# Performance work log

Hardware: AMD Instinct MI355X
Metric: run time of the kernel (lower is better)

## Reference

```python
import jax, jax.numpy as jnp
import numpy as np

K = 40  # GravNetConv k (hardcoded in PFNet7.forward's conv1)

def lrelu(x):
    # LeakyReLU(negative_slope=0.5)
    return jnp.where(x >= 0, x, 0.5 * x)

def lin(x, W, b=None):
    y = x @ W
    return y + b if b is not None else y


def setup_inputs() -> dict:
    key = jax.random.key(0)
    ks = jax.random.split(key, 24)
    N = 16384
    inp = {}
    inp["x0"] = jax.random.normal(ks[0], (N, 12), jnp.float32)
    inp["ygen"] = jax.random.normal(ks[1], (N, 6), jnp.float32)
    inp["ycand"] = jax.random.normal(ks[2], (N, 6), jnp.float32)
    inp["ygen_id"] = jax.random.randint(ks[3], (N,), 0, 6)
    inp["ycand_id"] = jax.random.randint(ks[4], (N,), 0, 6)

    def lp(k, din, dout):  # torch Linear default init (uniform +/- 1/sqrt(fan_in))
        s = float(1.0 / np.sqrt(din))
        kw, kb = jax.random.split(k)
        W = jax.random.uniform(kw, (din, dout), jnp.float32, -s, s)
        b = jax.random.uniform(kb, (dout,), jnp.float32, -s, s)
        return W, b

    inp["n1W0"], inp["n1b0"] = lp(ks[5], 12, 64)
    inp["n1W1"], inp["n1b1"] = lp(ks[6], 64, 64)
    inp["n1W2"], inp["n1b2"] = lp(ks[7], 64, 12)
    # GravNetConv: lin_s (space, 8), lin_h (propagate, 22), lin_out (12 + 2*22 -> 64)
    inp["gWs"], inp["gbs"] = lp(ks[8], 12, 8)
    inp["gWh"], inp["gbh"] = lp(ks[9], 12, 22)
    inp["gWo"], inp["gbo"] = lp(ks[10], 56, 64)
    # GraphConv: lin_rel (with bias), lin_root (no bias, PyG convention)
    inp["c2Wrel"], inp["c2brel"] = lp(ks[11], 64, 64)
    inp["c2Wroot"] = lp(ks[12], 64, 64)[0]
    inp["n2W0"], inp["n2b0"] = lp(ks[13], 64, 126)
    inp["n2W1"], inp["n2b1"] = lp(ks[14], 126, 126)
    inp["n2W2"], inp["n2b2"] = lp(ks[15], 126, 126)
    inp["n2W3"], inp["n2b3"] = lp(ks[16], 126, 6)
    inp["n3W0"], inp["n3b0"] = lp(ks[17], 82, 126)
    inp["n3W1"], inp["n3b1"] = lp(ks[18], 126, 126)
    inp["n3W2"], inp["n3b2"] = lp(ks[19], 126, 126)
    inp["n3W3"], inp["n3b3"] = lp(ks[20], 126, 6)
    return inp


def reference(x0, ygen, ycand, ygen_id, ycand_id,
              n1W0, n1b0, n1W1, n1b1, n1W2, n1b2,
              gWs, gbs, gWh, gbh, gWo, gbo,
              c2Wrel, c2brel, c2Wroot,
              n2W0, n2b0, n2W1, n2b1, n2W2, n2b2, n2W3, n2b3,
              n3W0, n3b0, n3W1, n3b1, n3W2, n3b2, n3W3, n3b3):
    N = x0.shape[0]
    # nn1 encoder
    x = lrelu(lin(x0, n1W0, n1b0))
    x = lrelu(lin(x, n1W1, n1b1))
    x = lrelu(lin(x, n1W2, n1b2))            # [N,12]
    # ---- GravNetConv: dynamic kNN graph in learned 8-dim space ----
    s = lin(x, gWs, gbs)                     # [N,8] spatial coords
    h = lin(x, gWh, gbh)                     # [N,22] propagated features
    sq = jnp.sum(s * s, axis=1)
    d2 = sq[:, None] + sq[None, :] - 2.0 * (s @ s.T)   # [N,N] squared dists
    ar = jnp.arange(N)
    d2 = d2.at[ar, ar].set(jnp.inf)          # knn_graph loop=False: no self edges
    negd2, idx = jax.lax.top_k(-d2, K)       # [N,K] k nearest neighbors
    w = jnp.exp(10.0 * negd2)                # edge_weight = exp(-10 * d^2)
    msg = h[idx] * w[..., None]              # [N,K,22] gathered messages
    agg = jnp.concatenate([msg.mean(axis=1), msg.max(axis=1)], axis=-1)  # [N,44]
    x = lin(jnp.concatenate([agg, x], axis=-1), gWo, gbo)  # [N,64]
    # ---- GraphConv on the same kNN graph (add-aggregation, edge-weighted) ----
    nbr = jnp.sum(x[idx] * w[..., None], axis=1)  # [N,64]
    x = lin(nbr, c2Wrel, c2brel) + x @ c2Wroot     # [N,64]
    # nn2: class id head
    y = lrelu(lin(x, n2W0, n2b0))
    y = lrelu(lin(y, n2W1, n2b1))
    y = lrelu(lin(y, n2W2, n2b2))
    cand_ids = lrelu(lin(y, n2W3, n2b3))     # [N,6]
    z = jnp.concatenate([x, cand_ids, x0], axis=-1)  # [N,82]
    z = lrelu(lin(z, n3W0, n3b0))
    z = lrelu(lin(z, n3W1, n3b1))
    z = lrelu(lin(z, n3W2, n3b2))
    cand_p4 = lrelu(lin(z, n3W3, n3b3))      # [N,6]
    return (cand_ids, cand_p4, ygen_id, ygen, ycand_id, ycand)
```

## Files before the change

### kernel.cpp

```cpp
#include <hip/hip_runtime.h>
#include <math.h>

static constexpr int KNN = 40;

__device__ __forceinline__ float lrelu_f(float v){ return v >= 0.f ? v : 0.5f*v; }

typedef _Float16 half8 __attribute__((ext_vector_type(8)));
typedef float    f32x4 __attribute__((ext_vector_type(4)));

__device__ __forceinline__ void gload16(const void* g, void* l){
    __builtin_amdgcn_global_load_lds((const __attribute__((address_space(1))) void*)g,
                                     (__attribute__((address_space(3))) void*)l, 16, 0, 0);
}

#define PAD_OFF_GWS   0
#define PAD_OFF_GWH   192
#define PAD_OFF_N1W2  576
#define PAD_OFF_N2W3  1600
#define PAD_OFF_N3W3  3616
#define PAD_TOTAL     5632

#define T_N2W0  0
#define T_N2W1  8192
#define T_N2W2  24576
#define T_N3W0  40960
#define T_N3W1  53248
#define T_N3W2  69632
#define T_TOTAL 86016

__global__ void pad_all(const float* gWs,const float* gWh,const float* n1W2,
                        const float* n2W3,const float* n3W3,
                        const float* n2W0,const float* n2W1,const float* n2W2,
                        const float* n3W0,const float* n3W1,const float* n3W2,
                        float* __restrict__ wp, _Float16* __restrict__ wt)
{
    int i = blockIdx.x*blockDim.x + threadIdx.x;
    if (i < PAD_TOTAL) {
        const float* src; int cols, sh, off;
        if      (i < PAD_OFF_GWH)  { src=gWs;  cols=8;  sh=4; off=PAD_OFF_GWS;  }
        else if (i < PAD_OFF_N1W2) { src=gWh;  cols=22; sh=5; off=PAD_OFF_GWH;  }
        else if (i < PAD_OFF_N2W3) { src=n1W2; cols=12; sh=4; off=PAD_OFF_N1W2; }
        else if (i < PAD_OFF_N3W3) { src=n2W3; cols=6;  sh=4; off=PAD_OFF_N2W3; }
        else                       { src=n3W3; cols=6;  sh=4; off=PAD_OFF_N3W3; }
        int li = i - off;
        int r = li >> sh, c = li & ((1<<sh)-1);
        wp[i] = (c < cols) ? src[r*cols + c] : 0.f;
        return;
    }
    int j = i - PAD_TOTAL;
    if (j >= T_TOTAL) return;
    const float* src; int KP, K, off;
    if      (j < T_N2W1) { src=n2W0; KP=64;  K=64;  off=T_N2W0; }
    else if (j < T_N2W2) { src=n2W1; KP=128; K=126; off=T_N2W1; }
    else if (j < T_N3W0) { src=n2W2; KP=128; K=126; off=T_N2W2; }
    else if (j < T_N3W1) { src=n3W0; KP=96;  K=82;  off=T_N3W0; }
    else if (j < T_N3W2) { src=n3W1; KP=128; K=126; off=T_N3W1; }
    else                 { src=n3W2; KP=128; K=126; off=T_N3W2; }
    int li = j - off;
    int n = li / KP, k = li - n*KP;
    float v = (n < 126 && k < K) ? src[k*126 + n] : 0.f;
    wt[j] = (_Float16)v;
}

template<int K, int NOUT, int WPITCH, bool RELU, int NTH>
__device__ __forceinline__
void lin8(const float* __restrict__ Xs, int xpitch,
          const float* __restrict__ W, const float* __restrict__ Bv,
          float* __restrict__ Y, int ypitch, int tid)
{
    constexpr int NP  = ((NOUT+7)/8)*8;
    constexpr int NCG = NP/8;
    constexpr int NW  = NTH/64;
    const int lane = tid & 63;
    for (int g0 = tid >> 6; g0 < NCG; g0 += NW) {
        const int cg = __builtin_amdgcn_readfirstlane(g0);
        float acc[8];
        #pragma unroll
        for (int j=0;j<8;++j){ int c=cg*8+j; acc[j] = (c < NOUT) ? Bv[c] : 0.f; }
        const float* xrow = &Xs[(long)lane*xpitch];
        const float* wp = &W[cg*8];
        #pragma unroll 4
        for (int k=0;k<K;++k){
            const float xv = xrow[k];
            const float4* w4 = reinterpret_cast<const float4*>(wp + (long)k*WPITCH);
            float4 a = w4[0], b = w4[1];
            acc[0]=fmaf(xv,a.x,acc[0]); acc[1]=fmaf(xv,a.y,acc[1]);
            acc[2]=fmaf(xv,a.z,acc[2]); acc[3]=fmaf(xv,a.w,acc[3]);
            acc[4]=fmaf(xv,b.x,acc[4]); acc[5]=fmaf(xv,b.y,acc[5]);
            acc[6]=fmaf(xv,b.z,acc[6]); acc[7]=fmaf(xv,b.w,acc[7]);
        }
        #pragma unroll
        for (int j=0;j<8;++j){
            int c = cg*8 + j;
            if (c < NOUT){ float v = acc[j]; if (RELU) v = lrelu_f(v); Y[(long)lane*ypitch + c] = v; }
        }
    }
    __syncthreads();
}

template<int K, int NOUT, int WPITCH, int NTH>
__device__ __forceinline__
void lin8_dual(const float* __restrict__ Xs, int xp, const float* __restrict__ X2s, int xp2,
               const float* __restrict__ W, const float* __restrict__ Bv, const float* __restrict__ W2,
               float* __restrict__ Y, int ypitch, int tid)
{
    constexpr int NP  = ((NOUT+7)/8)*8;
    constexpr int NCG = NP/8;
    constexpr int NW  = NTH/64;
    const int lane = tid & 63;
    for (int g0 = tid >> 6; g0 < NCG; g0 += NW) {
        const int cg = __builtin_amdgcn_readfirstlane(g0);
        float acc[8];
        #pragma unroll
        for (int j=0;j<8;++j){ int c=cg*8+j; acc[j] = (c < NOUT) ? Bv[c] : 0.f; }
        {
            const float* xrow = &Xs[(long)lane*xp];
            const float* wp = &W[cg*8];
            #pragma unroll 4
            for (int k=0;k<K;++k){
                const float xv = xrow[k];
                const float4* w4 = reinterpret_cast<const float4*>(wp + (long)k*WPITCH);
                float4 a = w4[0], b = w4[1];
                acc[0]=fmaf(xv,a.x,acc[0]); acc[1]=fmaf(xv,a.y,acc[1]);
                acc[2]=fmaf(xv,a.z,acc[2]); acc[3]=fmaf(xv,a.w,acc[3]);
                acc[4]=fmaf(xv,b.x,acc[4]); acc[5]=fmaf(xv,b.y,acc[5]);
                acc[6]=fmaf(xv,b.z,acc[6]); acc[7]=fmaf(xv,b.w,acc[7]);
            }
        }
        {
            const float* xrow = &X2s[(long)lane*xp2];
            const float* wp = &W2[cg*8];
            #pragma unroll 4
            for (int k=0;k<K;++k){
                const float xv = xrow[k];
                const float4* w4 = reinterpret_cast<const float4*>(wp + (long)k*WPITCH);
                float4 a = w4[0], b = w4[1];
                acc[0]=fmaf(xv,a.x,acc[0]); acc[1]=fmaf(xv,a.y,acc[1]);
                acc[2]=fmaf(xv,a.z,acc[2]); acc[3]=fmaf(xv,a.w,acc[3]);
                acc[4]=fmaf(xv,b.x,acc[4]); acc[5]=fmaf(xv,b.y,acc[5]);
                acc[6]=fmaf(xv,b.z,acc[6]); acc[7]=fmaf(xv,b.w,acc[7]);
            }
        }
        #pragma unroll
        for (int j=0;j<8;++j){
            int c = cg*8 + j;
            if (c < NOUT) Y[(long)lane*ypitch + c] = acc[j];
        }
    }
    __syncthreads();
}

__global__ __launch_bounds__(256)
void f1_encoder(const float* __restrict__ x0, const float* __restrict__ wp,
                const float* n1W0,const float* n1b0,const float* n1W1,const float* n1b1,
                const float* n1b2, const float* gbs, const float* gbh,
                float* __restrict__ x12g,
                _Float16* __restrict__ SA16, _Float16* __restrict__ SB16 ,
                float* __restrict__ hg )
{
    __shared__ float A1[64*65], A2[64*65], Ss[64*9];
    const int tid = threadIdx.x;
    const long row0 = (long)blockIdx.x*64;
    lin8<12,64,64,true,256>(x0+row0*12,12, n1W0, n1b0, A1,65, tid);
    lin8<64,64,64,true,256>(A1,65, n1W1, n1b1, A2,65, tid);
    lin8<64,12,16,true,256>(A2,65, wp+PAD_OFF_N1W2, n1b2, A1,13, tid);
    for (int i=tid;i<64*12;i+=256){ int r=i/12,c=i-r*12; x12g[(row0+r)*12+c]=A1[r*13+c]; }
    lin8<12,8,16,false,256>(A1,13, wp+PAD_OFF_GWS, gbs, Ss,9, tid);
    lin8<12,22,32,false,256>(A1,13, wp+PAD_OFF_GWH, gbh, hg+row0*32,32, tid);
    if (tid < 64) {
        const long node = row0 + tid;
        float sv[8]; float nq = 0.f;
        #pragma unroll
        for (int k=0;k<8;++k){ float v=Ss[tid*9+k]; sv[k]=v; nq=fmaf(v,v,nq); }
        _Float16 ch[8], clo[8];
        #pragma unroll
        for (int k=0;k<8;++k){ ch[k]=(_Float16)sv[k]; clo[k]=(_Float16)(sv[k]-(float)ch[k]); }
        _Float16 nh = (_Float16)nq, nl = (_Float16)(nq-(float)nh);
        const _Float16 one = (_Float16)1.f, zero = (_Float16)0.f;
        half8 a0,a1,a2,b0,b2;
        #pragma unroll
        for (int k=0;k<8;++k){
            a0[k]=ch[k]; a1[k]=clo[k]; a2[k]=ch[k];
            b0[k]=(_Float16)(-2.f*(float)ch[k]);
            b2[k]=(_Float16)(-2.f*(float)clo[k]);
        }
        half8 a3 = {nh, nl, one, one, zero, zero, zero, zero};
        half8 b3 = {one, one, nh, nl, zero, zero, zero, zero};
        half8* ap = (half8*)&SA16[(size_t)node*32];
        ap[0]=a0; ap[1]=a1; ap[2]=a2; ap[3]=a3;
        half8* bp = (half8*)&SB16[(size_t)node*40];
        bp[0]=b0; bp[1]=b0; bp[2]=b2; bp[3]=b3;
        bp[4]=half8{zero,zero,zero,zero,zero,zero,zero,zero};
    }
}

template<int C>
__device__ __forceinline__ unsigned dpp_umin(unsigned x){
    unsigned y = (unsigned)__builtin_amdgcn_update_dpp((int)x, (int)x, C, 0xf, 0xf, false);
    return x < y ? x : y;
}
__device__ __forceinline__ unsigned wave_umin64(unsigned x){
    x = dpp_umin<0x111>(x);
    x = dpp_umin<0x112>(x);
    x = dpp_umin<0x114>(x);
    x = dpp_umin<0x118>(x);
    x = dpp_umin<0x142>(x);
    x = dpp_umin<0x143>(x);
    return x;
}
__device__ __forceinline__ unsigned med3_u32(unsigned a, unsigned b, unsigned c){
    unsigned d;
    asm("v_med3_u32 %0, %1, %2, %3" : "=v"(d) : "v"(a), "v"(b), "v"(c));
    return d;
}

__global__ __launch_bounds__(512)
void knn_mfma(const _Float16* __restrict__ SA, const _Float16* __restrict__ SB,
              int* __restrict__ idx_out, float* __restrict__ w_out, int N)
{
    __shared__ __align__(16) _Float16 SBl[2][256*40];
    unsigned (*MRG)[128] = reinterpret_cast<unsigned(*)[128]>(&SBl[0][0]);
    const int tid  = threadIdx.x;
    const int lane = tid & 63;
    const int w    = tid >> 6;
    const int g    = w >> 2, qt = w & 3;
    const int col  = lane & 15, kg = lane >> 4;
    const int qb   = blockIdx.x*32 + g*16;
    const int qtile = qb >> 8;
    const int rhs0  = (qb & 255) + kg*4;

    half8 afrag = *(const half8*)&SA[(size_t)(qb + col)*32 + kg*8];
    unsigned s0[4], s1[4];
    #pragma unroll
    for (int r=0;r<4;++r){ s0[r]=0xFFFFFFFFu; s1[r]=0xFFFFFFFFu; }

    const int NT = N >> 8;
    {
        const char* gp = (const char*)SB;
        gload16(gp + (size_t)tid*16,        &SBl[0][(size_t)tid*8]);
        gload16(gp + (size_t)(tid+512)*16,  &SBl[0][(size_t)(tid+512)*8]);
        if (tid < 256) gload16(gp + (size_t)(tid+1024)*16, &SBl[0][(size_t)(tid+1024)*8]);
    }
    __syncthreads();
    #pragma unroll 1
    for (int t = 0; t < NT; ++t) {
        const int cur = t & 1;
        if (t+1 < NT) {
            const char* gp = (const char*)(SB + (size_t)(t+1)*256*40);
            _Float16* lp = SBl[cur^1];
            gload16(gp + (size_t)tid*16,        &lp[(size_t)tid*8]);
            gload16(gp + (size_t)(tid+512)*16,  &lp[(size_t)(tid+512)*8]);
            if (tid < 256) gload16(gp + (size_t)(tid+1024)*16, &lp[(size_t)(tid+1024)*8]);
        }
        const _Float16* tb = SBl[cur];
        if (t != qtile) {
            #pragma unroll
            for (int c3=0;c3<4;++c3){
                const int cl_ = (qt*4+c3)*16 + col;
                half8 b = *(const half8*)&tb[cl_*40 + kg*8];
                f32x4 acc = {0.f,0.f,0.f,0.f};
                acc = __builtin_amdgcn_mfma_f32_16x16x32_f16(afrag, b, acc, 0, 0, 0);
                const unsigned ib = (unsigned)((t<<2)|c3);
                #pragma unroll
                for (int r=0;r<4;++r){
                    float d2 = fmaxf(acc[r], 0.f);
                    unsigned key = (__float_as_uint(d2) & 0xFFFFFF00u) | ib;
                    unsigned lo = s0[r] < key ? s0[r] : key;
                    s1[r] = med3_u32(s0[r], s1[r], key);
                    s0[r] = lo;
                }
            }
        } else {
            #pragma unroll
            for (int c3=0;c3<4;++c3){
                const int cl_ = (qt*4+c3)*16 + col;
                half8 b = *(const half8*)&tb[cl_*40 + kg*8];
                f32x4 acc = {0.f,0.f,0.f,0.f};
                acc = __builtin_amdgcn_mfma_f32_16x16x32_f16(afrag, b, acc, 0, 0, 0);
                const unsigned ib = (unsigned)((t<<2)|c3);
                #pragma unroll
                for (int r=0;r<4;++r){
                    float d2 = fmaxf(acc[r], 0.f);
                    unsigned key = (__float_as_uint(d2) & 0xFFFFFF00u) | ib;
                    if (cl_ == rhs0 + r) key = 0xFFFFFFFFu;
                    unsigned lo = s0[r] < key ? s0[r] : key;
                    s1[r] = med3_u32(s0[r], s1[r], key);
                    s0[r] = lo;
                }
            }
        }
        __syncthreads();
    }

    #pragma unroll
    for (int r=0;r<4;++r){
        const int qloc = g*16 + kg*4 + r;
        MRG[qloc][qt*32 + col*2    ] = s0[r];
        MRG[qloc][qt*32 + col*2 + 1] = s1[r];
    }
    __syncthreads();

    const int myqt = lane >> 4, mycol = lane & 15;
    for (int qi=0; qi<4; ++qi){
        const int qloc = w*4 + qi;
        const long q = (long)blockIdx.x*32 + qloc;
        unsigned k0 = MRG[qloc][2*lane], k1 = MRG[qloc][2*lane+1];
        #pragma unroll 1
        for (int p=0;p<KNN;++p){
            unsigned lmin = k0 < k1 ? k0 : k1;
            unsigned red = wave_umin64(lmin);
            unsigned gm = (unsigned)__builtin_amdgcn_readlane((int)red, 63);
            unsigned long long bal = __ballot(lmin == gm);
            int owner = __ffsll((long long)bal) - 1;
            if (lane == owner){
                const int tt = (int)((gm>>2)&63u);
                const int c3 = (int)(gm & 3u);
                const int cand = tt*256 + (myqt*4+c3)*16 + mycol;
                const float d2 = __uint_as_float(gm & 0xFFFFFF00u);
                idx_out[q*KNN+p] = cand;
                w_out[q*KNN+p]   = expf(-10.f*d2);
                if (k0 == gm) k0 = k1;
                k1 = 0xFFFFFFFFu;
            }
        }
    }
}

__global__ __launch_bounds__(512)
void f2_agg(const float* __restrict__ hg , const int* __restrict__ idx,
            const float* __restrict__ wgt, const float* __restrict__ x12g,
            const float* gWo, const float* gbo, float* __restrict__ xg)
{
    __shared__ int   IDs[64*40];
    __shared__ float Wt[64*40];
    __shared__ float AGG[64*57];
    const int tid = threadIdx.x;
    const long row0 = (long)blockIdx.x*64;
    for (int i=tid;i<64*40;i+=512){ int r=i/40,k=i-r*40;
        IDs[i]=idx[(row0+r)*40+k]; Wt[i]=wgt[(row0+r)*40+k]; }
    for (int i=tid;i<64*12;i+=512){ int r=i/12,c=i-r*12; AGG[r*57+44+c]=x12g[(row0+r)*12+c]; }
    __syncthreads();
    {
        const int r = tid & 63, g = tid >> 6;
        const int f0 = g*4;
        const int nf = (f0 < 22) ? ((22-f0) < 4 ? (22-f0) : 4) : 0;
        float sm[4], mx[4];
        #pragma unroll
        for (int u=0;u<4;++u){ sm[u]=0.f; mx[u]=-INFINITY; }
        if (nf > 0) {
            #pragma unroll 1
            for (int k=0;k<40;++k){
                int j = IDs[r*40+k]; float wv = Wt[r*40+k];
                float4 h0 = *reinterpret_cast<const float4*>(&hg[(long)j*32 + f0]);
                float hv[4] = {h0.x,h0.y,h0.z,h0.w};
                #pragma unroll
                for (int u=0;u<4;++u){ float m = hv[u]*wv; sm[u]+=m; mx[u]=fmaxf(mx[u],m); }
            }
            #pragma unroll
            for (int u=0;u<4;++u) if (u<nf){ AGG[r*57+f0+u]=sm[u]*(1.f/40.f); AGG[r*57+22+f0+u]=mx[u]; }
        }
    }
    __syncthreads();
    lin8<56,64,64,false,512>(AGG,57, gWo, gbo, xg+row0*64,64, tid);
}

__global__ __launch_bounds__(512)
void f3_graphconv(const float* __restrict__ xgin, const int* __restrict__ idx,
                  const float* __restrict__ wgt,
                  const float* c2Wrel, const float* c2brel, const float* c2Wroot,
                  float* __restrict__ xc)
{
    __shared__ int   IDs[64*40];
    __shared__ float Wt[64*40];
    __shared__ float NB[64*65], XGs[64*65];
    const int tid = threadIdx.x;
    const long row0 = (long)blockIdx.x*64;
    for (int i=tid;i<64*40;i+=512){ int r=i/40,k=i-r*40;
        IDs[i]=idx[(row0+r)*40+k]; Wt[i]=wgt[(row0+r)*40+k]; }
    for (int i=tid;i<64*64;i+=512){ int r=i>>6,c=i&63; XGs[r*65+c]=xgin[(row0+r)*64+c]; }
    __syncthreads();
    {
        const int r = tid & 63, g = tid >> 6;
        float acc[8];
        #pragma unroll
        for (int j=0;j<8;++j) acc[j]=0.f;
        #pragma unroll 1
        for (int k=0;k<40;++k){
            int j = IDs[r*40+k]; float wv = Wt[r*40+k];
            const float4* xp = reinterpret_cast<const float4*>(&xgin[(long)j*64 + g*8]);
            float4 v0 = xp[0], v1 = xp[1];
            acc[0]=fmaf(v0.x,wv,acc[0]); acc[1]=fmaf(v0.y,wv,acc[1]);
            acc[2]=fmaf(v0.z,wv,acc[2]); acc[3]=fmaf(v0.w,wv,acc[3]);
            acc[4]=fmaf(v1.x,wv,acc[4]); acc[5]=fmaf(v1.y,wv,acc[5]);
            acc[6]=fmaf(v1.z,wv,acc[6]); acc[7]=fmaf(v1.w,wv,acc[7]);
        }
        #pragma unroll
        for (int j=0;j<8;++j) NB[r*65 + g*8 + j] = acc[j];
    }
    __syncthreads();
    lin8_dual<64,64,64,512>(NB,65, XGs,65, c2Wrel,c2brel,c2Wroot, xc+row0*64,64, tid);
}

template<int KP>
__device__ __forceinline__
void mfma_layer(const _Float16* __restrict__ Xl, const _Float16* __restrict__ WTg,
                _Float16* __restrict__ Wl,
                const float* __restrict__ Bv, _Float16* __restrict__ Yl, int tid)
{
    {
        const half8* src = reinterpret_cast<const half8*>(WTg);
        half8* dst = reinterpret_cast<half8*>(Wl);
        constexpr int CHUNKS = 128*KP/8;
        #pragma unroll
        for (int i = tid; i < CHUNKS; i += 1024) dst[i] = src[i];
    }
    __syncthreads();
    const int lane = tid & 63;
    const int wid  = __builtin_amdgcn_readfirstlane(tid >> 6);
    const int m   = wid & 3;
    const int nb  = wid >> 2;
    const int c15 = lane & 15;
    const int kg  = lane >> 4;
    f32x4 acc0 = {0.f,0.f,0.f,0.f};
    f32x4 acc1 = {0.f,0.f,0.f,0.f};
    const _Float16* xb = &Xl[(m*16 + c15)*136];
    const _Float16* w0 = &Wl[(nb*16 + c15)*KP];
    const _Float16* w1 = &Wl[((nb+4)*16 + c15)*KP];
    #pragma unroll
    for (int ks = 0; ks < KP/32; ++ks) {
        const int kb = kg*8 + ks*32;
        half8 a  = *reinterpret_cast<const half8*>(&xb[kb]);
        half8 b0 = *reinterpret_cast<const half8*>(&w0[kb]);
        half8 b1 = *reinterpret_cast<const half8*>(&w1[kb]);
        acc0 = __builtin_amdgcn_mfma_f32_16x16x32_f16(a, b0, acc0, 0, 0, 0);
        acc1 = __builtin_amdgcn_mfma_f32_16x16x32_f16(a, b1, acc1, 0, 0, 0);
    }
    const int drow = m*16 + kg*4;
    const int c0 = nb*16 + c15;
    const int c1 = (nb+4)*16 + c15;
    #pragma unroll
    for (int r = 0; r < 4; ++r) {
        float v0 = (c0 < 126) ? lrelu_f(acc0[r] + Bv[c0]) : 0.f;
        float v1 = (c1 < 126) ? lrelu_f(acc1[r] + Bv[c1]) : 0.f;
        Yl[(drow+r)*136 + c0] = (_Float16)v0;
        Yl[(drow+r)*136 + c1] = (_Float16)v1;
    }
    __syncthreads();
}

__device__ __forceinline__
void lin_out6h(const _Float16* __restrict__ Xs, const float* __restrict__ Wp,
               float* __restrict__ Wl6, const float* __restrict__ Bv,
               float* __restrict__ Y, int ypitch, int tid)
{
    for (int i = tid; i < 126*8; i += 1024) {
        int k = i >> 3, c = i & 7;
        Wl6[i] = Wp[k*16 + c];
    }
    __syncthreads();
    if (tid < 64*6) {
        const int r = tid / 6, c = tid - r*6;
        float acc = Bv[c];
        const _Float16* xrow = &Xs[r*136];
        #pragma unroll 4
        for (int k=0;k<126;++k) acc = fmaf((float)xrow[k], Wl6[k*8+c], acc);
        Y[(long)r*ypitch + c] = lrelu_f(acc);
    }
    __syncthreads();
}

__global__ __launch_bounds__(1024)
void f45_mfma(const float* __restrict__ xc, const float* __restrict__ x0,
              const float* __restrict__ wp, const _Float16* __restrict__ wt,
              const float* A_b0,const float* A_b1,const float* A_b2,const float* A_b3,
              const float* B_b0,const float* B_b1,const float* B_b2,const float* B_b3,
              float* __restrict__ outIds, float* __restrict__ outP4)
{
    __shared__ __align__(16) _Float16 bufA[64*136];
    __shared__ __align__(16) _Float16 bufB[64*136];
    __shared__ __align__(16) _Float16 Wl[128*128];
    __shared__ float IDS[64*6];
    const int tid = threadIdx.x;
    const long row0 = (long)blockIdx.x*64;
    for (int i=tid;i<64*64;i+=1024){ int r=i>>6,c=i&63;
        bufA[r*136+c] = (_Float16)xc[(row0+r)*64+c]; }
    __syncthreads();
    mfma_layer<64>(bufA, wt+T_N2W0, Wl, A_b0, bufB, tid);
    mfma_layer<128>(bufB, wt+T_N2W1, Wl, A_b1, bufA, tid);
    mfma_layer<128>(bufA, wt+T_N2W2, Wl, A_b2, bufB, tid);
    lin_out6h(bufB, wp+PAD_OFF_N2W3, (float*)Wl, A_b3, IDS, 6, tid);
    for (int i=tid;i<64*6;i+=1024){ int r=i/6,c=i-r*6; outIds[(row0+r)*6+c]=IDS[i]; }
    for (int i=tid;i<64*96;i+=1024){
        int r=i/96, c=i-r*96;
        float v;
        if (c < 64)      v = xc[(row0+r)*64 + c];
        else if (c < 70) v = IDS[r*6 + (c-64)];
        else if (c < 82) v = x0[(row0+r)*12 + (c-70)];
        else             v = 0.f;
        bufA[r*136+c] = (_Float16)v;
    }
    __syncthreads();
    mfma_layer<96>(bufA, wt+T_N3W0, Wl, B_b0, bufB, tid);
    mfma_layer<128>(bufB, wt+T_N3W1, Wl, B_b1, bufA, tid);
    mfma_layer<128>(bufA, wt+T_N3W2, Wl, B_b2, bufB, tid);
    lin_out6h(bufB, wp+PAD_OFF_N3W3, (float*)Wl, B_b3, outP4+row0*6, 6, tid);
}

__global__ void copyout_kernel(const int* __restrict__ gid, const float* __restrict__ gy,
                               const int* __restrict__ cid, const float* __restrict__ cy,
                               float* __restrict__ out, int N)
{
    long i = (long)blockIdx.x*blockDim.x + threadIdx.x;
    long n = N;
    if (i < n)            out[12*n + i]         = (float)gid[i];
    else if (i < 7*n)     out[13*n + (i - n)]   = gy[i - n];
    else if (i < 8*n)     out[19*n + (i - 7*n)] = (float)cid[i - 7*n];
    else if (i < 14*n)    out[20*n + (i - 8*n)] = cy[i - 8*n];
}

extern "C" void kernel_launch(void* const* d_in, const int* in_sizes, int n_in,
                              void* d_out, int out_size, void* d_ws, size_t ws_size,
                              hipStream_t stream)
{
    const float* x0     = (const float*)d_in[0];
    const float* ygen   = (const float*)d_in[1];
    const float* ycand  = (const float*)d_in[2];
    const int*   ygenid = (const int*)d_in[3];
    const int*   ycandid= (const int*)d_in[4];
    const float* n1W0=(const float*)d_in[5],  *n1b0=(const float*)d_in[6];
    const float* n1W1=(const float*)d_in[7],  *n1b1=(const float*)d_in[8];
    const float* n1W2=(const float*)d_in[9],  *n1b2=(const float*)d_in[10];
    const float* gWs =(const float*)d_in[11], *gbs =(const float*)d_in[12];
    const float* gWh =(const float*)d_in[13], *gbh =(const float*)d_in[14];
    const float* gWo =(const float*)d_in[15], *gbo =(const float*)d_in[16];
    const float* c2Wrel=(const float*)d_in[17], *c2brel=(const float*)d_in[18];
    const float* c2Wroot=(const float*)d_in[19];
    const float* n2W0=(const float*)d_in[20], *n2b0=(const float*)d_in[21];
    const float* n2W1=(const float*)d_in[22], *n2b1=(const float*)d_in[23];
    const float* n2W2=(const float*)d_in[24], *n2b2=(const float*)d_in[25];
    const float* n2W3=(const float*)d_in[26], *n2b3=(const float*)d_in[27];
    const float* n3W0=(const float*)d_in[28], *n3b0=(const float*)d_in[29];
    const float* n3W1=(const float*)d_in[30], *n3b1=(const float*)d_in[31];
    const float* n3W2=(const float*)d_in[32], *n3b2=(const float*)d_in[33];
    const float* n3W3=(const float*)d_in[34], *n3b3=(const float*)d_in[35];

    const int N = in_sizes[0] / 12;
    float* ws = (float*)d_ws;
    size_t off = 0;
    auto alloc = [&](size_t cnt){ float* p = ws + off; off += cnt; return p; };
    float* padw = alloc(PAD_TOTAL);
    _Float16* wt16 = (_Float16*)alloc((T_TOTAL+1)/2 + 8);
    float* x12  = alloc((size_t)N*12);
    _Float16* SA16 = (_Float16*)alloc((size_t)N*16);
    _Float16* SB16 = (_Float16*)alloc((size_t)N*20);
    float* h    = alloc((size_t)N*32);
    int*   idxb = (int*)alloc((size_t)N*KNN);
    float* wb   = alloc((size_t)N*KNN);
    float* xg   = alloc((size_t)N*64);
    float* xc   = alloc((size_t)N*64);
    (void)ws_size; (void)n_in; (void)out_size;

    float* outF = (float*)d_out;
    const int GB = N / 64;

    pad_all<<<(PAD_TOTAL+T_TOTAL+255)/256,256,0,stream>>>(gWs,gWh,n1W2,n2W3,n3W3,
                                                          n2W0,n2W1,n2W2,n3W0,n3W1,n3W2,
                                                          padw, wt16);
    f1_encoder<<<GB,256,0,stream>>>(x0, padw, n1W0,n1b0, n1W1,n1b1, n1b2,
                                    gbs, gbh, x12, SA16, SB16, h);
    knn_mfma<<<N/32, 512, 0, stream>>>(SA16, SB16, idxb, wb, N);
    f2_agg<<<GB,512,0,stream>>>(h, idxb, wb, x12, gWo, gbo, xg);
    f3_graphconv<<<GB,512,0,stream>>>(xg, idxb, wb, c2Wrel, c2brel, c2Wroot, xc);
    f45_mfma<<<GB,1024,0,stream>>>(xc, x0, padw, wt16,
                                   n2b0,n2b1,n2b2,n2b3, n3b0,n3b1,n3b2,n3b3,
                                   outF, outF + (size_t)N*6);
    copyout_kernel<<<(14*N+255)/256,256,0,stream>>>(ygenid, ygen, ycandid, ycand, outF, N);
}
```

Before: 232.8 us.

## Split kNN scan across two blocks per query group with separate merge kernel

The kNN distance scan is split so each query group is handled by two blocks, each scanning half of the candidate tiles, and their per-lane top-2 candidates are written to a global partial buffer. A new merge kernel runs one wave per query and selects the 40 nearest from 256 candidates, writing all results at once via lane-indexed stores. The sort key now encodes the full 14-bit candidate index, which lowers distance precision. It adds a kernel launch and an N*256 partial buffer, and hardcodes 64 tiles (N=16384) and 14-bit indices.

```diff
diff --git a/kernel.cpp b/kernel.cpp
--- a/kernel.cpp
+++ b/kernel.cpp
@@ -215,37 +215,37 @@
 }
 
 __global__ __launch_bounds__(512)
-void knn_mfma(const _Float16* __restrict__ SA, const _Float16* __restrict__ SB,
-              int* __restrict__ idx_out, float* __restrict__ w_out, int N)
+void knn_scan(const _Float16* __restrict__ SA, const _Float16* __restrict__ SB,
+              unsigned* __restrict__ part, int N)
 {
     __shared__ __align__(16) _Float16 SBl[2][256*40];
-    unsigned (*MRG)[128] = reinterpret_cast<unsigned(*)[128]>(&SBl[0][0]);
     const int tid  = threadIdx.x;
     const int lane = tid & 63;
     const int w    = tid >> 6;
     const int g    = w >> 2, qt = w & 3;
     const int col  = lane & 15, kg = lane >> 4;
-    const int qb   = blockIdx.x*32 + g*16;
+    const int qg   = blockIdx.x >> 1, half = blockIdx.x & 1;
+    const int qb   = qg*32 + g*16;
     const int qtile = qb >> 8;
     const int rhs0  = (qb & 255) + kg*4;
+    const int T0 = half*32;
 
     half8 afrag = *(const half8*)&SA[(size_t)(qb + col)*32 + kg*8];
     unsigned s0[4], s1[4];
     #pragma unroll
     for (int r=0;r<4;++r){ s0[r]=0xFFFFFFFFu; s1[r]=0xFFFFFFFFu; }
 
-    const int NT = N >> 8;
     {
-        const char* gp = (const char*)SB;
+        const char* gp = (const char*)(SB + (size_t)T0*256*40);
         gload16(gp + (size_t)tid*16,        &SBl[0][(size_t)tid*8]);
         gload16(gp + (size_t)(tid+512)*16,  &SBl[0][(size_t)(tid+512)*8]);
         if (tid < 256) gload16(gp + (size_t)(tid+1024)*16, &SBl[0][(size_t)(tid+1024)*8]);
     }
     __syncthreads();
     #pragma unroll 1
-    for (int t = 0; t < NT; ++t) {
+    for (int t = T0; t < T0+32; ++t) {
         const int cur = t & 1;
-        if (t+1 < NT) {
+        if (t+1 < T0+32) {
             const char* gp = (const char*)(SB + (size_t)(t+1)*256*40);
             _Float16* lp = SBl[cur^1];
             gload16(gp + (size_t)tid*16,        &lp[(size_t)tid*8]);
@@ -260,11 +260,11 @@
                 half8 b = *(const half8*)&tb[cl_*40 + kg*8];
                 f32x4 acc = {0.f,0.f,0.f,0.f};
                 acc = __builtin_amdgcn_mfma_f32_16x16x32_f16(afrag, b, acc, 0, 0, 0);
-                const unsigned ib = (unsigned)((t<<2)|c3);
+                const unsigned ib = (unsigned)((t<<8)|cl_);
                 #pragma unroll
                 for (int r=0;r<4;++r){
                     float d2 = fmaxf(acc[r], 0.f);
-                    unsigned key = (__float_as_uint(d2) & 0xFFFFFF00u) | ib;
+                    unsigned key = (__float_as_uint(d2) & 0xFFFFC000u) | ib;
                     unsigned lo = s0[r] < key ? s0[r] : key;
                     s1[r] = med3_u32(s0[r], s1[r], key);
                     s0[r] = lo;
@@ -277,11 +277,11 @@
                 half8 b = *(const half8*)&tb[cl_*40 + kg*8];
                 f32x4 acc = {0.f,0.f,0.f,0.f};
                 acc = __builtin_amdgcn_mfma_f32_16x16x32_f16(afrag, b, acc, 0, 0, 0);
-                const unsigned ib = (unsigned)((t<<2)|c3);
+                const unsigned ib = (unsigned)((t<<8)|cl_);
                 #pragma unroll
                 for (int r=0;r<4;++r){
                     float d2 = fmaxf(acc[r], 0.f);
-                    unsigned key = (__float_as_uint(d2) & 0xFFFFFF00u) | ib;
+                    unsigned key = (__float_as_uint(d2) & 0xFFFFC000u) | ib;
                     if (cl_ == rhs0 + r) key = 0xFFFFFFFFu;
                     unsigned lo = s0[r] < key ? s0[r] : key;
                     s1[r] = med3_u32(s0[r], s1[r], key);
@@ -294,35 +294,42 @@
 
     #pragma unroll
     for (int r=0;r<4;++r){
-        const int qloc = g*16 + kg*4 + r;
-        MRG[qloc][qt*32 + col*2    ] = s0[r];
-        MRG[qloc][qt*32 + col*2 + 1] = s1[r];
-    }
-    __syncthreads();
-
-    const int myqt = lane >> 4, mycol = lane & 15;
-    for (int qi=0; qi<4; ++qi){
-        const int qloc = w*4 + qi;
-        const long q = (long)blockIdx.x*32 + qloc;
-        unsigned k0 = MRG[qloc][2*lane], k1 = MRG[qloc][2*lane+1];
-        #pragma unroll 1
-        for (int p=0;p<KNN;++p){
-            unsigned lmin = k0 < k1 ? k0 : k1;
-            unsigned red = wave_umin64(lmin);
-            unsigned gm = (unsigned)__builtin_amdgcn_readlane((int)red, 63);
-            unsigned long long bal = __ballot(lmin == gm);
-            int owner = __ffsll((long long)bal) - 1;
-            if (lane == owner){
-                const int tt = (int)((gm>>2)&63u);
-                const int c3 = (int)(gm & 3u);
-                const int cand = tt*256 + (myqt*4+c3)*16 + mycol;
-                const float d2 = __uint_as_float(gm & 0xFFFFFF00u);
-                idx_out[q*KNN+p] = cand;
-                w_out[q*KNN+p]   = expf(-10.f*d2);
-                if (k0 == gm) k0 = k1;
-                k1 = 0xFFFFFFFFu;
-            }
-        }
+        const long q = (long)qg*32 + g*16 + kg*4 + r;
+        unsigned* pp = &part[((size_t)q*2 + half)*128 + qt*32 + col*2];
+        pp[0] = s0[r]; pp[1] = s1[r];
+    }
+}
+
+__global__ __launch_bounds__(512)
+void knn_merge(const unsigned* __restrict__ part,
+               int* __restrict__ idx_out, float* __restrict__ w_out)
+{
+    const int lane = threadIdx.x & 63, w = threadIdx.x >> 6;
+    const long q = (long)blockIdx.x*8 + w;
+    const uint4 kk = *reinterpret_cast<const uint4*>(&part[(size_t)q*256 + lane*4]);
+    unsigned k0=kk.x, k1=kk.y, k2=kk.z, k3=kk.w;
+    unsigned saved = 0;
+    #pragma unroll 1
+    for (int p=0;p<KNN;++p){
+        unsigned a = k0 < k1 ? k0 : k1;
+        unsigned b = k2 < k3 ? k2 : k3;
+        unsigned lmin = a < b ? a : b;
+        unsigned red = wave_umin64(lmin);
+        unsigned gm = (unsigned)__builtin_amdgcn_readlane((int)red, 63);
+        unsigned long long bal = __ballot(lmin == gm);
+        int owner = __ffsll((long long)bal) - 1;
+        if (lane == owner){
+            if      (k0 == gm) k0 = 0xFFFFFFFFu;
+            else if (k1 == gm) k1 = 0xFFFFFFFFu;
+            else if (k2 == gm) k2 = 0xFFFFFFFFu;
+            else               k3 = 0xFFFFFFFFu;
+        }
+        if (lane == p) saved = gm;
+    }
+    if (lane < KNN){
+        idx_out[q*KNN + lane] = (int)(saved & 16383u);
+        const float d2 = __uint_as_float(saved & 0xFFFFC000u);
+        w_out[q*KNN + lane] = expf(-10.f*d2);
     }
 }
 
@@ -554,6 +561,7 @@
     _Float16* SA16 = (_Float16*)alloc((size_t)N*16);
     _Float16* SB16 = (_Float16*)alloc((size_t)N*20);
     float* h    = alloc((size_t)N*32);
+    unsigned* part = (unsigned*)alloc((size_t)N*256);
     int*   idxb = (int*)alloc((size_t)N*KNN);
     float* wb   = alloc((size_t)N*KNN);
     float* xg   = alloc((size_t)N*64);
@@ -568,7 +576,8 @@
                                                           padw, wt16);
     f1_encoder<<<GB,256,0,stream>>>(x0, padw, n1W0,n1b0, n1W1,n1b1, n1b2,
                                     gbs, gbh, x12, SA16, SB16, h);
-    knn_mfma<<<N/32, 512, 0, stream>>>(SA16, SB16, idxb, wb, N);
+    knn_scan<<<(N/32)*2, 512, 0, stream>>>(SA16, SB16, part, N);
+    knn_merge<<<N/8, 512, 0, stream>>>(part, idxb, wb);
     f2_agg<<<GB,512,0,stream>>>(h, idxb, wb, x12, gWo, gbo, xg);
     f3_graphconv<<<GB,512,0,stream>>>(xg, idxb, wb, c2Wrel, c2brel, c2Wroot, xc);
     f45_mfma<<<GB,1024,0,stream>>>(xc, x0, padw, wt16,
```

Result: faster. 215.4 us (-7.5%).
